# Kernel tuning notes

Hardware: AMD Instinct MI355X
Metric: run time of the kernel (lower is better)

Reference implementation:

```python
import jax, jax.numpy as jnp
from jax import lax
import numpy as np

D_IN = 512    # inputdim
HID = 128     # hiddendim
D_INNER = 2 * HID   # 256
D_PROJ = 2 * D_INNER  # 512
N_STATE = 16
R_DT = 8      # ceil(128/16)
B, H, W = 8, 32, 32


def _layernorm(y, g, b):
    mu = y.mean(-1, keepdims=True)
    var = ((y - mu) ** 2).mean(-1, keepdims=True)
    return (y - mu) / jnp.sqrt(var + 1e-5) * g + b


def _ssm(x, xw, dtw, dtb, Al, Dv, g, be):
    # x: [B, D, L] -> y: [B, L, D]  (Mamba selective scan, delta_softplus=True)
    Bb, D, L = x.shape
    n = Al.shape[1]
    xd = jnp.einsum('bdl,kd->blk', x, xw)             # [B,L,R+2N]
    dts = xd[..., :R_DT]
    Bs = xd[..., R_DT:R_DT + n]                        # [B,L,N]
    Cs = xd[..., R_DT + n:]                            # [B,L,N]
    delta = jax.nn.softplus(jnp.einsum('blr,dr->bld', dts, dtw) + dtb)  # [B,L,D]
    A = -jnp.exp(Al)                                   # [D,N]
    xt = x.transpose(0, 2, 1)                          # [B,L,D]
    dA = jnp.exp(delta[..., None] * A)                 # [B,L,D,N]
    dBx = delta[..., None] * Bs[:, :, None, :] * xt[..., None]  # [B,L,D,N]

    def step(h, inp):
        da, dbx, c = inp
        h = h * da + dbx
        return h, jnp.einsum('bdn,bn->bd', h, c)

    h0 = jnp.zeros((Bb, D, n), x.dtype)
    _, ys = lax.scan(step, h0, (dA.transpose(1, 0, 2, 3),
                                dBx.transpose(1, 0, 2, 3),
                                Cs.transpose(1, 0, 2)))
    y = ys.transpose(1, 0, 2) + xt * Dv                # [B,L,D]
    return _layernorm(y, g, be)


def _up2(y, h, w):
    Bb, L, C = y.shape
    img = y.transpose(0, 2, 1).reshape(Bb, C, h, w)
    img = jnp.repeat(jnp.repeat(img, 2, axis=2), 2, axis=3)
    return img.reshape(Bb, C, 4 * L).transpose(0, 2, 1)


def _conv1x1(x, w, b):
    return jnp.einsum('bchw,oc->bohw', x, w) + b[None, :, None, None]


def _conv2s2(x, w, b):
    out = lax.conv_general_dilated(x, w, (2, 2), 'VALID',
                                   dimension_numbers=('NCHW', 'OIHW', 'NCHW'))
    return out + b[None, :, None, None]


def _forward(input_f, in_w, in_b, c1_w, c1_b, c2_w, c2_b, c3_w, c3_b, out_w, out_b,
             xw1, dtw1, dtb1, Al1, Dv1, g1, be1,
             xw2, dtw2, dtb2, Al2, Dv2, g2, be2,
             xw3, dtw3, dtb3, Al3, Dv3, g3, be3):
    xz = _conv1x1(input_f, in_w, in_b)
    x, z = jnp.split(xz, 2, axis=1)
    f1 = _conv1x1(x, c1_w, c1_b)                      # [B,256,H,W]
    f2 = _conv2s2(f1, c2_w, c2_b)                     # [B,256,H/2,W/2]
    f3 = _conv2s2(f2, c3_w, c3_b)                     # [B,256,H/4,W/4]

    Bb, C, h3, w3 = f3.shape
    fx3 = f3.reshape(Bb, C, h3 * w3)
    y3 = _ssm(fx3, xw3, dtw3, dtb3, Al3, Dv3, g3, be3) + \
         jnp.flip(_ssm(jnp.flip(fx3, -1), xw3, dtw3, dtb3, Al3, Dv3, g3, be3), 1)
    y2_ = _up2(y3, h3, w3)

    _, _, h2, w2 = f2.shape
    fx2 = f2.reshape(Bb, C, h2 * w2)
    y2 = _ssm(fx2, xw2, dtw2, dtb2, Al2, Dv2, g2, be2) + \
         jnp.flip(_ssm(jnp.flip(fx2, -1), xw2, dtw2, dtb2, Al2, Dv2, g2, be2), 1) + y2_
    y1_ = _up2(y2, h2, w2)

    _, _, h1, w1 = f1.shape
    fx1 = f1.reshape(Bb, C, h1 * w1)
    # NOTE: source uses fssm1 forward and fssm2 on the flipped sequence
    y1 = _ssm(fx1, xw1, dtw1, dtb1, Al1, Dv1, g1, be1) + \
         jnp.flip(_ssm(jnp.flip(fx1, -1), xw2, dtw2, dtb2, Al2, Dv2, g2, be2), 1) + y1_

    out1 = y1.transpose(0, 2, 1).reshape(Bb, C, h1, w1)
    out = out1 * jax.nn.silu(z)
    return _conv1x1(out, out_w, out_b)


def setup_inputs() -> dict:
    key = jax.random.key(0)
    ks = iter(jax.random.split(key, 64))
    def nrm(shape, s=0.05):
        return (jax.random.normal(next(ks), shape, dtype=jnp.float32) * s)
    inp = {
        'input_f': jax.random.normal(next(ks), (B, D_IN, H, W), dtype=jnp.float32),
        'in_w': nrm((D_PROJ, D_IN)), 'in_b': nrm((D_PROJ,)),
        'c1_w': nrm((D_INNER, D_INNER)), 'c1_b': nrm((D_INNER,)),
        'c2_w': nrm((D_INNER, D_INNER, 2, 2)), 'c2_b': nrm((D_INNER,)),
        'c3_w': nrm((D_INNER, D_INNER, 2, 2)), 'c3_b': nrm((D_INNER,)),
        'out_w': nrm((D_IN, D_INNER)), 'out_b': nrm((D_IN,)),
    }
    Al = jnp.log(jnp.tile(jnp.arange(1, N_STATE + 1, dtype=jnp.float32), (D_INNER, 1)))
    for i in (1, 2, 3):
        inp[f'xw{i}'] = nrm((R_DT + 2 * N_STATE, D_INNER))
        inp[f'dtw{i}'] = nrm((D_INNER, R_DT), s=R_DT ** -0.5)
        inp[f'dtb{i}'] = nrm((D_INNER,)) - 4.0   # inv-softplus of small dt
        inp[f'Al{i}'] = Al
        inp[f'Dv{i}'] = jnp.ones((D_INNER,), jnp.float32)
        inp[f'g{i}'] = jnp.ones((D_INNER,), jnp.float32)
        inp[f'be{i}'] = jnp.zeros((D_INNER,), jnp.float32)
    return inp


def reference(input_f, in_w, in_b, c1_w, c1_b, c2_w, c2_b, c3_w, c3_b, out_w, out_b,
              xw1, dtw1, dtb1, Al1, Dv1, g1, be1,
              xw2, dtw2, dtb2, Al2, Dv2, g2, be2,
              xw3, dtw3, dtb3, Al3, Dv3, g3, be3):
    return _forward(input_f, in_w, in_b, c1_w, c1_b, c2_w, c2_b, c3_w, c3_b, out_w, out_b,
                    xw1, dtw1, dtb1, Al1, Dv1, g1, be1,
                    xw2, dtw2, dtb2, Al2, Dv2, g2, be2,
                    xw3, dtw3, dtb3, Al3, Dv3, g3, be3)
```

## Files before the change

### kernel.cpp

```cpp
#include <hip/hip_runtime.h>
#include <cstddef>

#define DEV static __device__ __forceinline__

typedef __attribute__((ext_vector_type(8))) short short8;
typedef __attribute__((ext_vector_type(4))) float floatx4;

DEV float siluf(float v) { return v / (1.f + expf(-v)); }

DEV unsigned short f2bf(float f) {
  unsigned int u = __float_as_uint(f);
  u += 0x7fff + ((u >> 16) & 1);
  return (unsigned short)(u >> 16);
}
DEV float bf2f(unsigned short u) {
  return __uint_as_float(((unsigned int)u) << 16);
}
DEV float4 bf2f4(ushort4 v) {
  return make_float4(bf2f(v.x), bf2f(v.y), bf2f(v.z), bf2f(v.w));
}

template <int CTRL>
DEV float qadd(float v) {
  int s = __builtin_amdgcn_update_dpp(__float_as_int(v), __float_as_int(v),
                                      CTRL, 0xF, 0xF, false);
  return v + __int_as_float(s);
}

__global__ __launch_bounds__(256) void prep_k(
    const float* __restrict__ in_w, const float* __restrict__ c1_w,
    const float* __restrict__ c2_w, const float* __restrict__ c3_w,
    const float* __restrict__ out_w, const float* __restrict__ xw1,
    const float* __restrict__ xw2, const float* __restrict__ xw3,
    unsigned short* __restrict__ wsW,
    const float* __restrict__ input_f, unsigned short* __restrict__ inT)
{
  __shared__ float tile[32][33];
  int bid = blockIdx.x;
  int t = threadIdx.x;
  if (bid < 3960) {
    int gid = bid * 256 + t;
    float v;
    if      (gid < 262144)  v = in_w[gid];
    else if (gid < 327680)  v = c1_w[gid - 262144];
    else if (gid < 589824)  {
      int off = gid - 327680;
      int o = off >> 10, kk = off & 1023, ij = kk >> 8, c = kk & 255;
      v = c2_w[o * 1024 + c * 4 + ij];
    }
    else if (gid < 851968)  {
      int off = gid - 589824;
      int o = off >> 10, kk = off & 1023, ij = kk >> 8, c = kk & 255;
      v = c3_w[o * 1024 + c * 4 + ij];
    }
    else if (gid < 983040)  v = out_w[gid - 851968];
    else if (gid < 993280)  v = xw1[gid - 983040];
    else if (gid < 1003520) v = xw2[gid - 993280];
    else                    v = xw3[gid - 1003520];
    wsW[gid] = f2bf(v);
  } else {
    int idx = bid - 3960;
    int b = idx >> 9, blk = idx & 511;
    int pt = blk & 31, ct = blk >> 5;
    int p0 = pt * 32, c0 = ct * 32;
    int r = t >> 5, cc = t & 31;
#pragma unroll
    for (int i = 0; i < 4; i++) {
      int row = r + 8 * i;
      tile[row][cc] = input_f[((size_t)b * 512 + c0 + row) * 1024 + p0 + cc];
    }
    __syncthreads();
#pragma unroll
    for (int i = 0; i < 4; i++) {
      int row = r + 8 * i;
      inT[((size_t)b * 1024 + p0 + row) * 512 + c0 + cc] = f2bf(tile[cc][row]);
    }
  }
}

template <int EPI>
DEV void mgemm_body(const unsigned short* __restrict__ A, long long sA,
                    const unsigned short* __restrict__ B, long long sB,
                    const float* __restrict__ bias,
                    void* __restrict__ O1, void* __restrict__ O2,
                    int M, int N, int K, int Mt, int Nt, int bid)
{
  __shared__ __align__(16) unsigned short Ab[2 * 128 * 40];
  __shared__ __align__(16) unsigned short Bb[2 * 128 * 40];
  int tiles = Mt * Nt;
  int bb = bid / tiles;
  int rr = bid - bb * tiles;
  int m0 = (rr / Nt) * 128;
  int n0 = (rr % Nt) * 128;
  const unsigned short* Ap = A + (size_t)bb * sA;
  const unsigned short* Bp = B + (size_t)bb * sB;

  int t = threadIdx.x;
  int lane = t & 63;
  int wm = ((t >> 7) & 1) * 64;
  int wn = ((t >> 6) & 1) * 64;
  int l15 = lane & 15, quad = lane >> 4;

  int srow = t >> 1;
  int shalf = (t & 1) * 16;
  int arow = m0 + srow; if (arow > M - 1) arow = M - 1;
  int brow = n0 + srow; if (brow > N - 1) brow = N - 1;
  const unsigned short* ap = Ap + (size_t)arow * K + shalf;
  const unsigned short* bp = Bp + (size_t)brow * K + shalf;
  unsigned short* as = &Ab[srow * 40 + shalf];
  unsigned short* bs = &Bb[srow * 40 + shalf];

  floatx4 acc[4][4] = {};

  uint4 a0 = *(const uint4*)(ap);
  uint4 a1 = *(const uint4*)(ap + 8);
  uint4 b0 = *(const uint4*)(bp);
  uint4 b1 = *(const uint4*)(bp + 8);
// ... 3 lines not shown
  int cur = 0;
  for (int k0 = 0; k0 < K; k0 += 32) {
    bool last = (k0 + 32 >= K);
    if (!last) {
      a0 = *(const uint4*)(ap + k0 + 32);
      a1 = *(const uint4*)(ap + k0 + 40);
      b0 = *(const uint4*)(bp + k0 + 32);
      b1 = *(const uint4*)(bp + k0 + 40);
    }
    int co = cur * 5120;
    short8 af[4], bfr[4];
#pragma unroll
    for (int i = 0; i < 4; i++)
      af[i] = *(const short8*)&Ab[co + (wm + i * 16 + l15) * 40 + quad * 8];
#pragma unroll
    for (int j = 0; j < 4; j++)
      bfr[j] = *(const short8*)&Bb[co + (wn + j * 16 + l15) * 40 + quad * 8];
#pragma unroll
    for (int i = 0; i < 4; i++)
#pragma unroll
      for (int j = 0; j < 4; j++)
        acc[i][j] = __builtin_amdgcn_mfma_f32_16x16x32_bf16(af[i], bfr[j],
                                                            acc[i][j], 0, 0, 0);
    if (!last) {
      int no = 5120 - co;
      *(uint4*)(as + no) = a0; *(uint4*)(as + no + 8) = a1;
      *(uint4*)(bs + no) = b0; *(uint4*)(bs + no + 8) = b1;
      __syncthreads();
      cur ^= 1;
    }
  }

  if (EPI == 1) {
    unsigned short* Yt = (unsigned short*)O1;
    unsigned short* Ys = (unsigned short*)O2;
    float bn[4]; int nn[4];
#pragma unroll
    for (int j = 0; j < 4; j++) { nn[j] = n0 + wn + j * 16 + l15; bn[j] = bias[nn[j]]; }
#pragma unroll
    for (int i = 0; i < 4; i++) {
      int pixb = m0 + wm + i * 16 + quad * 4;
#pragma unroll
      for (int j = 0; j < 4; j++) {
        int n = nn[j];
        if (n < 256) {
#pragma unroll
          for (int r = 0; r < 4; r++)
            Yt[((size_t)bb * 1024 + pixb + r) * 256 + n] = f2bf(acc[i][j][r] + bn[j]);
        } else {
#pragma unroll
          for (int r = 0; r < 4; r++)
            Ys[((size_t)bb * 1024 + pixb + r) * 256 + (n - 256)] =
                f2bf(siluf(acc[i][j][r] + bn[j]));
        }
      }
    }
  } else {
#pragma unroll
    for (int i = 0; i < 4; i++) {
      int m = m0 + wm + i * 16 + quad * 4;
#pragma unroll
      for (int j = 0; j < 4; j++) {
        int n = n0 + wn + j * 16 + l15;
        if (m < M && n < N) {
          float vr[4];
#pragma unroll
          for (int r = 0; r < 4; r++)
            vr[r] = acc[i][j][r] + (bias ? bias[m + r] : 0.f);
          if (EPI == 0) {
            float* Y0 = (float*)O1;
            float* yp = &Y0[((size_t)bb * M + m) * N + n];
#pragma unroll
            for (int r = 0; r < 4; r++) yp[(size_t)r * N] = vr[r];
          } else {
            unsigned short* Y0b = (unsigned short*)O1;
            unsigned short* Yt  = (unsigned short*)O2;
#pragma unroll
            for (int r = 0; r < 4; r++)
              Y0b[((size_t)bb * M + m + r) * N + n] = f2bf(vr[r]);
            ushort4 o;
            o.x = f2bf(vr[0]); o.y = f2bf(vr[1]); o.z = f2bf(vr[2]); o.w = f2bf(vr[3]);
            *(ushort4*)&Yt[((size_t)bb * N + n) * M + m] = o;
          }
        }
      }
    }
  }
}

template <int EPI>
__global__ __launch_bounds__(256) void mgemm_k(
    const unsigned short* __restrict__ A, long long sA,
    const unsigned short* __restrict__ B, long long sB,
    const float* __restrict__ bias, void* __restrict__ O1, void* __restrict__ O2,
    int M, int N, int K, int Mt, int Nt)
{
  mgemm_body<EPI>(A, sA, B, sB, bias, O1, O2, M, N, K, Mt, Nt, blockIdx.x);
}

__global__ __launch_bounds__(256) void cgemm_k(
    const unsigned short* __restrict__ A,
    const unsigned short* __restrict__ B, long long sB,
    const float* __restrict__ bias,
    unsigned short* __restrict__ O1, unsigned short* __restrict__ O2,
    int M, int N, int K, int Mt, int Nt)
{
  __shared__ __align__(16) unsigned short Ab[2][64 * 72];
  __shared__ __align__(16) unsigned short Bb[2][32 * 72];
  int bid = blockIdx.x;
  int tiles = Mt * Nt;
  int bb = bid / tiles;
  int rr = bid - bb * tiles;
  int m0 = (rr / Nt) * 64;
  int n0 = (rr % Nt) * 32;
  const unsigned short* Bp = B + (size_t)bb * sB;

  int t = threadIdx.x, lane = t & 63;
  int wm = ((t >> 7) & 1) * 32;
  int wn = ((t >> 6) & 1) * 16;
  int l15 = lane & 15, quad = lane >> 4;

  int ar = t >> 2, ac = (t & 3) * 16;
  int brc = (t >> 2) & 31, bc = (t & 3) * 16;
  const unsigned short* apc = A + (size_t)(m0 + ar) * K + ac;
  const unsigned short* bpc = Bp + (size_t)(n0 + brc) * K + bc;

  floatx4 acc2[2] = {};

  uint4 av0 = *(const uint4*)(apc);
  uint4 av1 = *(const uint4*)(apc + 8);
// ... 39 lines not shown
      unsigned short* asn = &Ab[cur ^ 1][0] + ar * 72 + ac;
      *(uint4*)asn = av0; *(uint4*)(asn + 8) = av1;
      if (t < 128) {
        unsigned short* bsn = &Bb[cur ^ 1][0] + brc * 72 + bc;
        *(uint4*)bsn = bv0; *(uint4*)(bsn + 8) = bv1;
      }
      __syncthreads();
      cur ^= 1;
    }
  }

#pragma unroll
  for (int i = 0; i < 2; i++) {
    int m = m0 + wm + i * 16 + quad * 4;
    int n = n0 + wn + l15;
    float vr[4];
#pragma unroll
    for (int r = 0; r < 4; r++) vr[r] = acc2[i][r] + bias[m + r];
#pragma unroll
    for (int r = 0; r < 4; r++)
      O1[((size_t)bb * M + m + r) * N + n] = f2bf(vr[r]);
    ushort4 o;
    o.x = f2bf(vr[0]); o.y = f2bf(vr[1]); o.z = f2bf(vr[2]); o.w = f2bf(vr[3]);
    *(ushort4*)&O2[((size_t)bb * N + n) * M + m] = o;
  }
}

__global__ __launch_bounds__(256) void fat1_k(
    const unsigned short* __restrict__ w_xw12, const unsigned short* __restrict__ f1t,
    float* __restrict__ xd12, unsigned short* __restrict__ ic2)
{
  int bid = blockIdx.x;
  if (bid < 64) {
    mgemm_body<0>(w_xw12, 0, f1t, 1024 * 256, nullptr, xd12, nullptr,
                  80, 1024, 256, 1, 8, bid);
  } else {
    int idx = (bid - 64) * 256 + threadIdx.x;
    int cs = idx & 31, ij = (idx >> 5) & 3, n = (idx >> 7) & 255, b = idx >> 15;
    int i = ij >> 1, j = ij & 1;
    int y = n >> 4, x = n & 15;
    int pix = (2 * y + i) * 32 + 2 * x + j;
    uint4 v = *(const uint4*)&f1t[((size_t)b * 1024 + pix) * 256 + cs * 8];
    *(uint4*)&ic2[((size_t)b * 256 + n) * 1024 + ij * 256 + cs * 8] = v;
  }
}

__global__ __launch_bounds__(256) void fat2_k(
    const unsigned short* __restrict__ w_xw2, const unsigned short* __restrict__ f2t,
    float* __restrict__ xd2, unsigned short* __restrict__ ic3)
{
  int bid = blockIdx.x;
  if (bid < 16) {
    mgemm_body<0>(w_xw2, 0, f2t, 256 * 256, nullptr, xd2, nullptr,
                  40, 256, 256, 1, 2, bid);
  } else {
    int idx = (bid - 16) * 256 + threadIdx.x;
    int cs = idx & 31, ij = (idx >> 5) & 3, n = (idx >> 7) & 63, b = idx >> 13;
    int i = ij >> 1, j = ij & 1;
    int y = n >> 3, x = n & 7;
    int pix = (2 * y + i) * 16 + 2 * x + j;
    uint4 v = *(const uint4*)&f2t[((size_t)b * 256 + pix) * 256 + cs * 8];
    *(uint4*)&ic3[((size_t)b * 64 + n) * 1024 + ij * 256 + cs * 8] = v;
  }
}

__global__ __launch_bounds__(256) void post_all_k(
    const float* __restrict__ xd12, const float* __restrict__ xd2,
    const float* __restrict__ xd3,
    const float* __restrict__ dtw1, const float* __restrict__ dtb1,
    const float* __restrict__ dtw2, const float* __restrict__ dtb2,
    const float* __restrict__ dtw3, const float* __restrict__ dtb3,
    float* __restrict__ d1f, float* __restrict__ bc1f,
    float* __restrict__ d1b, float* __restrict__ bc1b,
    float* __restrict__ d2g, float* __restrict__ bc2,
    float* __restrict__ d3g, float* __restrict__ bc3)
{
  int bid = blockIdx.x;
  const float* xd; int bstride, L; const float *dtw, *dtb; float *dg, *bg;
  int lt, b;
  if (bid < 512) {
    int r = bid; lt = r & 63; b = r >> 6;
    xd = xd12; bstride = 80 * 1024; L = 1024; dtw = dtw1; dtb = dtb1; dg = d1f; bg = bc1f;
  } else if (bid < 1024) {
    int r = bid - 512; lt = r & 63; b = r >> 6;
    xd = xd12 + 40 * 1024; bstride = 80 * 1024; L = 1024; dtw = dtw2; dtb = dtb2; dg = d1b; bg = bc1b;
  } else if (bid < 1152) {
// ... 14 lines not shown
    int tt = t - 128;
    int c = tt >> 2, seg = tt & 3;
    float4 v = *(const float4*)&xb[(size_t)(8 + c) * L + seg * 4];
    *(float4*)&bg[((size_t)b * 32 + c) * L + l0 + seg * 4] = v;
  }
  __syncthreads();
  int d = t;
  float dtwv[8];
#pragma unroll
  for (int r = 0; r < 8; r++) dtwv[r] = dtw[d * 8 + r];
  float dtbv = dtb[d];
  float spv[16];
#pragma unroll
  for (int l = 0; l < 16; l++) {
    float s = dtbv;
#pragma unroll
    for (int r = 0; r < 8; r++) s += dl[r][l] * dtwv[r];
    spv[l] = fmaxf(s, 0.f) + log1pf(expf(-fabsf(s)));
  }
  float* dout = dg + ((size_t)b * 256 + d) * L + l0;
#pragma unroll
  for (int i = 0; i < 4; i++)
    *(float4*)&dout[4 * i] = make_float4(spv[4 * i], spv[4 * i + 1],
                                         spv[4 * i + 2], spv[4 * i + 3]);
}

#define SCAN_STEPA(DVV, DXV, BVV) {                     \
    float e_ = __builtin_amdgcn_exp2f((DVV) * A2);      \
    h = h * e_ + (BVV) * (DXV);                         \
    S += (DVV); }

__global__ __launch_bounds__(256) void scanA_k(
    const unsigned short* __restrict__ f1b, const unsigned short* __restrict__ f2b,
    const float* __restrict__ d1f, const float* __restrict__ bc1f,
    const float* __restrict__ d1b, const float* __restrict__ bc1b,
    const float* __restrict__ d2,  const float* __restrict__ bc2,
    const float* __restrict__ Al1, const float* __restrict__ Al2,
    float* __restrict__ cP, float* __restrict__ cQ)
{
  __shared__ __align__(16) float lds[48][68];
  int bid = blockIdx.x;
  int sid, tseg, L; const unsigned short* xin; const float *dlp, *bcp, *Alp;
  if (bid < 4096) {
    sid = bid >> 4; tseg = bid & 15; L = 1024; xin = f1b;
    if (((sid >> 4) & 1) == 0) { dlp = d1f; bcp = bc1f; Alp = Al1; }
    else                       { dlp = d1b; bcp = bc1b; Alp = Al2; }
  } else {
    int idx = bid - 4096; sid = idx >> 2; tseg = idx & 3; L = 256;
    xin = f2b; dlp = d2; bcp = bc2; Alp = Al2;
  }
  int b = sid >> 5, dir = (sid >> 4) & 1, g = sid & 15;
  int t = threadIdx.x, n = t & 15, dloc = t >> 4, d = g * 16 + dloc;
  int mbase = dir ? (L - 64 * (tseg + 1)) : 64 * tseg;

  int r0 = t >> 4, cs = t & 15;
  {
    const float* p0 = dlp + ((size_t)b * 256 + g * 16 + r0) * L + mbase;
    const unsigned short* p1 = xin + ((size_t)b * 256 + g * 16 + r0) * L + mbase;
    const float* p2 = bcp + ((size_t)b * 32 + r0) * L + mbase;
    float4 v0 = *(const float4*)(p0 + cs * 4);
    float4 xf = bf2f4(*(const ushort4*)(p1 + cs * 4));
    float4 v2 = *(const float4*)(p2 + cs * 4);
    float4 dx = make_float4(v0.x * xf.x, v0.y * xf.y, v0.z * xf.z, v0.w * xf.w);
    *(float4*)&lds[r0][cs * 4]      = v0;
    *(float4*)&lds[16 + r0][cs * 4] = dx;
    *(float4*)&lds[32 + r0][cs * 4] = v2;
  }
  __syncthreads();

  float A2 = -expf(Alp[d * 16 + n]) * 1.442695040888963f;
  float h = 0.f, S = 0.f;
  if (dir == 0) {
#pragma unroll
    for (int g4 = 0; g4 < 16; g4++) {
      int cb = 4 * g4;
      float4 dv4 = *(const float4*)&lds[dloc][cb];
      float4 dx4 = *(const float4*)&lds[16 + dloc][cb];
      float4 bv4 = *(const float4*)&lds[32 + n][cb];
      SCAN_STEPA(dv4.x, dx4.x, bv4.x);
      SCAN_STEPA(dv4.y, dx4.y, bv4.y);
      SCAN_STEPA(dv4.z, dx4.z, bv4.z);
      SCAN_STEPA(dv4.w, dx4.w, bv4.w);
    }
  } else {
#pragma unroll
    for (int g4 = 0; g4 < 16; g4++) {
      int cb = 60 - 4 * g4;
      float4 dv4 = *(const float4*)&lds[dloc][cb];
      float4 dx4 = *(const float4*)&lds[16 + dloc][cb];
      float4 bv4 = *(const float4*)&lds[32 + n][cb];
      SCAN_STEPA(dv4.w, dx4.w, bv4.w);
      SCAN_STEPA(dv4.z, dx4.z, bv4.z);
      SCAN_STEPA(dv4.y, dx4.y, bv4.y);
      SCAN_STEPA(dv4.x, dx4.x, bv4.x);
    }
  }
  cP[(size_t)bid * 256 + t] = __builtin_amdgcn_exp2f(S * A2);
  cQ[(size_t)bid * 256 + t] = h;
}

#define QSTEP(DS, XU, CI, II) {                                         \
    float4 bv = *(const float4*)&ld_b[CI][n0];                          \
    float4 cv = *(const float4*)&ld_c[CI][n0];                          \
    float xs_ = bf2f(XU) * (DS);                                        \
    float4 e_;                                                          \
    e_.x = __builtin_amdgcn_exp2f((DS) * A4.x);                         \
    e_.y = __builtin_amdgcn_exp2f((DS) * A4.y);                         \
    e_.z = __builtin_amdgcn_exp2f((DS) * A4.z);                         \
    e_.w = __builtin_amdgcn_exp2f((DS) * A4.w);                         \
    h4.x = h4.x * e_.x + bv.x * xs_;                                    \
    h4.y = h4.y * e_.y + bv.y * xs_;                                    \
    h4.z = h4.z * e_.z + bv.z * xs_;                                    \
    h4.w = h4.w * e_.w + bv.w * xs_;                                    \
    float pp_ = h4.x * cv.x + h4.y * cv.y + h4.z * cv.z + h4.w * cv.w;  \
    pp_ = qadd<0xB1>(pp_);                                              \
    pp_ = qadd<0x4E>(pp_);                                              \
    ysel = (nq == (II)) ? pp_ : ysel; }

DEV float4 pcomb(float4 P, float4 h, float4 Q) {
  return make_float4(P.x * h.x + Q.x, P.y * h.y + Q.y,
                     P.z * h.z + Q.z, P.w * h.w + Q.w);
}

__global__ __launch_bounds__(256) void scanC_k(
    const unsigned short* __restrict__ f1b, const unsigned short* __restrict__ f2b,
    const unsigned short* __restrict__ f3b,
    const float* __restrict__ d1f, const float* __restrict__ bc1f,
    const float* __restrict__ d1b, const float* __restrict__ bc1b,
    const float* __restrict__ d2,  const float* __restrict__ bc2,
    const float* __restrict__ d3,  const float* __restrict__ bc3,
    float* __restrict__ y1f, float* __restrict__ y1b,
    float* __restrict__ y2f, float* __restrict__ y2b,
    float* __restrict__ y3f, float* __restrict__ y3b,
    const float* __restrict__ Al1, const float* __restrict__ Dv1,
    const float* __restrict__ Al2, const float* __restrict__ Dv2,
    const float* __restrict__ Al3, const float* __restrict__ Dv3,
    const float* __restrict__ cP, const float* __restrict__ cQ)
{
  __shared__ __align__(16) float ld_d[64][68];
  __shared__ __align__(16) unsigned short ld_xs[64][72];
  __shared__ __align__(16) float ld_b[64][20];
  __shared__ __align__(16) float ld_c[64][20];

  int bid = blockIdx.x;
  int b, dir, g4, tseg, L, lvl;
  const unsigned short* xin; const float *dlp, *bcp, *Alp, *Dvp; float* yo;
  if (bid < 1024) {
    b = bid >> 7; dir = (bid >> 6) & 1; g4 = (bid >> 4) & 3; tseg = bid & 15;
    L = 1024; xin = f1b; lvl = 1;
    if (dir == 0) { dlp = d1f; bcp = bc1f; Alp = Al1; Dvp = Dv1; yo = y1f; }
    else          { dlp = d1b; bcp = bc1b; Alp = Al2; Dvp = Dv2; yo = y1b; }
  } else if (bid < 1280) {
    int idx = bid - 1024;
    b = idx >> 5; dir = (idx >> 4) & 1; g4 = (idx >> 2) & 3; tseg = idx & 3;
    L = 256; xin = f2b; lvl = 2;
    dlp = d2; bcp = bc2; Alp = Al2; Dvp = Dv2; yo = dir ? y2b : y2f;
  } else {
    int idx = bid - 1280;
    b = idx >> 3; dir = (idx >> 2) & 1; g4 = idx & 3; tseg = 0;
    L = 64; xin = f3b; lvl = 3;
    dlp = d3; bcp = bc3; Alp = Al3; Dvp = Dv3; yo = dir ? y3b : y3f;
  }
  int mbase = dir ? (L - 64 * (tseg + 1)) : 64 * tseg;
  int t = threadIdx.x;
  int dl = t >> 2, nq = t & 3, n0 = nq * 4;
  int d = g4 * 64 + dl;

  {
    int rr = t >> 2, q = t & 3;
    const float* dr = dlp + ((size_t)b * 256 + g4 * 64 + rr) * L + mbase;
    const unsigned short* xr = xin + ((size_t)b * 256 + g4 * 64 + rr) * L + mbase;
#pragma unroll
    for (int j = 0; j < 4; ++j) {
      int c = q * 4 + 16 * j;
      float4 dv = *(const float4*)(dr + c);
      ushort4 xu = *(const ushort4*)(xr + c);
      *(float4*)&ld_d[rr][c] = dv;
      *(ushort4*)&ld_xs[rr][c] = xu;
    }
    int nn = t >> 4, c4 = t & 15;
    const float* br = bcp + ((size_t)b * 32 + nn) * L + mbase + c4 * 4;
    const float* cr = br + (size_t)16 * L;
    float4 bv = *(const float4*)br;
    float4 cv = *(const float4*)cr;
    ld_b[c4 * 4 + 0][nn] = bv.x; ld_b[c4 * 4 + 1][nn] = bv.y;
    ld_b[c4 * 4 + 2][nn] = bv.z; ld_b[c4 * 4 + 3][nn] = bv.w;
    ld_c[c4 * 4 + 0][nn] = cv.x; ld_c[c4 * 4 + 1][nn] = cv.y;
    ld_c[c4 * 4 + 2][nn] = cv.z; ld_c[c4 * 4 + 3][nn] = cv.w;
  }

  float4 A4;
  A4.x = -expf(Alp[d * 16 + n0 + 0]) * 1.442695040888963f;
  A4.y = -expf(Alp[d * 16 + n0 + 1]) * 1.442695040888963f;
  A4.z = -expf(Alp[d * 16 + n0 + 2]) * 1.442695040888963f;
  A4.w = -expf(Alp[d * 16 + n0 + 3]) * 1.442695040888963f;
  float Dvv = Dvp[d];

  float4 h4 = make_float4(0.f, 0.f, 0.f, 0.f);
  if (tseg > 0) {
    int gold = g4 * 4 + (dl >> 4);
    int soff = (lvl == 1) ? (b * 32 + dir * 16 + gold) * 16
                          : 4096 + (b * 32 + dir * 16 + gold) * 4;
    size_t cbase = (size_t)soff * 256 + (size_t)((dl & 15) * 16 + n0);
    int s = 0;
    for (; s + 4 <= tseg; s += 4) {
      const float* p = &cP[cbase + (size_t)s * 256];
      const float* q = &cQ[cbase + (size_t)s * 256];
      float4 P0 = *(const float4*)(p);       float4 Q0 = *(const float4*)(q);
      float4 P1 = *(const float4*)(p + 256); float4 Q1 = *(const float4*)(q + 256);
      float4 P2 = *(const float4*)(p + 512); float4 Q2 = *(const float4*)(q + 512);
      float4 P3 = *(const float4*)(p + 768); float4 Q3 = *(const float4*)(q + 768);
      h4 = pcomb(P0, h4, Q0); h4 = pcomb(P1, h4, Q1);
      h4 = pcomb(P2, h4, Q2); h4 = pcomb(P3, h4, Q3);
    }
    for (; s < tseg; ++s) {
      float4 P = *(const float4*)&cP[cbase + (size_t)s * 256];
      float4 Q = *(const float4*)&cQ[cbase + (size_t)s * 256];
      h4 = pcomb(P, h4, Q);
    }
  }
  __syncthreads();

  float* ybase = yo + ((size_t)b * L + mbase) * 256 + d;
  if (dir == 0) {
#pragma unroll
    for (int p = 0; p < 4; ++p) {
      float yk[4];
#pragma unroll
      for (int j = 0; j < 4; ++j) {
        int cb = 16 * p + 4 * j;
        float4 dv4 = *(const float4*)&ld_d[dl][cb];
        ushort4 xu4 = *(const ushort4*)&ld_xs[dl][cb];
        float ysel = 0.f;
        QSTEP(dv4.x, xu4.x, cb + 0, 0);
        QSTEP(dv4.y, xu4.y, cb + 1, 1);
        QSTEP(dv4.z, xu4.z, cb + 2, 2);
        QSTEP(dv4.w, xu4.w, cb + 3, 3);
        yk[j] = ysel;
      }
#pragma unroll
      for (int j = 0; j < 4; ++j) {
        int cst = 16 * p + 4 * j + nq;
        float xv = bf2f(ld_xs[dl][cst]);
        ybase[(size_t)cst * 256] = yk[j] + xv * Dvv;
      }
    }
  } else {
#pragma unroll
    for (int p = 0; p < 4; ++p) {
      float yk[4];
#pragma unroll
      for (int j = 0; j < 4; ++j) {
        int cb = 60 - 16 * p - 4 * j;
        float4 dv4 = *(const float4*)&ld_d[dl][cb];
        ushort4 xu4 = *(const ushort4*)&ld_xs[dl][cb];
        float ysel = 0.f;
        QSTEP(dv4.w, xu4.w, cb + 3, 0);
        QSTEP(dv4.z, xu4.z, cb + 2, 1);
        QSTEP(dv4.y, xu4.y, cb + 1, 2);
        QSTEP(dv4.x, xu4.x, cb + 0, 3);
        yk[j] = ysel;
      }
#pragma unroll
      for (int j = 0; j < 4; ++j) {
        int cst = 60 - 16 * p - 4 * j + (3 - nq);
        float xv = bf2f(ld_xs[dl][cst]);
        ybase[(size_t)cst * 256] = yk[j] + xv * Dvv;
      }
    }
  }
}

template <int OUTBF>
__global__ __launch_bounds__(256) void ln_combine(
    const float* __restrict__ yf, const float* __restrict__ yb,
    const float* __restrict__ gf, const float* __restrict__ bef,
    const float* __restrict__ gb, const float* __restrict__ beb,
    const float* __restrict__ up, int Wc,
    const unsigned short* __restrict__ szb, void* __restrict__ outv,
    int L, int Lsh, int Wfsh)
{
  int t = threadIdx.x;
  int row = blockIdx.x * 4 + (t >> 6);
  int lane = t & 63;
  int b = row >> Lsh, l = row & (L - 1);
  size_t base = (size_t)row * 256 + lane * 4;
  float4 vf = *(const float4*)&yf[base];
  float4 vb = *(const float4*)&yb[base];
  float4 s;
  s.x = vf.x + vf.y + vf.z + vf.w;
  s.y = vf.x * vf.x + vf.y * vf.y + vf.z * vf.z + vf.w * vf.w;
  s.z = vb.x + vb.y + vb.z + vb.w;
  s.w = vb.x * vb.x + vb.y * vb.y + vb.z * vb.z + vb.w * vb.w;
#pragma unroll
  for (int m = 1; m < 64; m <<= 1) {
    s.x += __shfl_xor(s.x, m);
    s.y += __shfl_xor(s.y, m);
    s.z += __shfl_xor(s.z, m);
// ... 43 lines not shown
  const float* c1_w  = (const float*)d_in[3];
  const float* c1_b  = (const float*)d_in[4];
  const float* c2_w  = (const float*)d_in[5];
  const float* c2_b  = (const float*)d_in[6];
  const float* c3_w  = (const float*)d_in[7];
  const float* c3_b  = (const float*)d_in[8];
  const float* out_w = (const float*)d_in[9];
  const float* out_b = (const float*)d_in[10];
  const float* xw1  = (const float*)d_in[11];
  const float* dtw1 = (const float*)d_in[12];
  const float* dtb1 = (const float*)d_in[13];
  const float* Al1  = (const float*)d_in[14];
  const float* Dv1  = (const float*)d_in[15];
  const float* g1   = (const float*)d_in[16];
  const float* be1  = (const float*)d_in[17];
  const float* xw2  = (const float*)d_in[18];
  const float* dtw2 = (const float*)d_in[19];
  const float* dtb2 = (const float*)d_in[20];
  const float* Al2  = (const float*)d_in[21];
  const float* Dv2  = (const float*)d_in[22];
  const float* g2   = (const float*)d_in[23];
  const float* be2  = (const float*)d_in[24];
  const float* xw3  = (const float*)d_in[25];
  const float* dtw3 = (const float*)d_in[26];
  const float* dtb3 = (const float*)d_in[27];
  const float* Al3  = (const float*)d_in[28];
  const float* Dv3  = (const float*)d_in[29];
  const float* g3   = (const float*)d_in[30];
  const float* be3  = (const float*)d_in[31];

  float* ws = (float*)d_ws;
  constexpr size_t M1 = 2097152;
  float* d1f = ws;
  unsigned short* xt = (unsigned short*)(ws + M1);
  float* y1f = ws + M1;
  unsigned short* szb = (unsigned short*)(ws + 2 * M1);
  unsigned short* f1b = (unsigned short*)(ws + 3 * M1);
  unsigned short* G = (unsigned short*)(ws + 3 * M1) + 2097152;
  float* d1b = ws + 4 * M1;
  unsigned short* inT = (unsigned short*)(ws + 5 * M1);
  unsigned short* ic2 = inT;
  unsigned short* f1t = inT + 2097152;
  unsigned short* ic3 = f1t;
  float* y1b = ws + 5 * M1;
  size_t o = 6 * M1;
  unsigned short* f2b = (unsigned short*)(ws + o); o += 524288;
  unsigned short* f3b = (unsigned short*)(ws + o); o += 131072;
  float* bc1f = ws + o; o += 262144;
  float* bc1b = ws + o; o += 262144;
  float* d2   = ws + o; o += 524288;
  float* bc2  = ws + o; o += 65536;
  float* d3   = ws + o; o += 131072;
  float* bc3  = ws + o; o += 16384;
  float* y2f  = ws + o; o += 524288;
  float* y2b  = ws + o; o += 524288;
  float* y3f  = ws + o; o += 131072;
  float* y3b  = ws + o; o += 131072;
  float* y3c  = ws + o; o += 131072;
  float* y2c  = ws + o; o += 524288;
  float* cP   = ws + o; o += 1310720;
  float* cQ   = ws + o; o += 1310720;
  unsigned short* wsW = (unsigned short*)(ws + o); o += 506880;
  float* xd12 = cP;
  float* xd2  = cP + 655360;
  float* xd3  = cP + 737280;
  unsigned short* f2t = (unsigned short*)cQ;
  unsigned short* f3t = (unsigned short*)(cQ + 262144);
  unsigned short* w_in   = wsW;
  unsigned short* w_c1   = wsW + 262144;
  unsigned short* w_c2   = wsW + 327680;
  unsigned short* w_c3   = wsW + 589824;
  unsigned short* w_out  = wsW + 851968;
  unsigned short* w_xw12 = wsW + 983040;
  unsigned short* w_xw2  = wsW + 993280;
  unsigned short* w_xw3  = wsW + 1003520;

  dim3 blk(256);

  prep_k<<<dim3(8056), blk, 0, stream>>>(in_w, c1_w, c2_w, c3_w, out_w,
                                         xw1, xw2, xw3, wsW, input_f, inT);
  mgemm_k<1><<<dim3(256), blk, 0, stream>>>(inT, 1024 * 512, w_in, 0, in_b,
                                            xt, szb, 1024, 512, 512, 8, 4);
  mgemm_k<3><<<dim3(128), blk, 0, stream>>>(w_c1, 0, xt, 1024 * 256, c1_b,
                                            f1b, f1t, 256, 1024, 256, 2, 8);
  fat1_k<<<dim3(1088), blk, 0, stream>>>(w_xw12, f1t, xd12, ic2);
  cgemm_k<<<dim3(256), blk, 0, stream>>>(w_c2, ic2, 256 * 1024, c2_b,
                                         f2b, f2t, 256, 256, 1024, 4, 8);
  fat2_k<<<dim3(272), blk, 0, stream>>>(w_xw2, f2t, xd2, ic3);
  cgemm_k<<<dim3(64), blk, 0, stream>>>(w_c3, ic3, 64 * 1024, c3_b,
                                        f3b, f3t, 256, 64, 1024, 4, 2);
  mgemm_k<0><<<dim3(8), blk, 0, stream>>>(w_xw3, 0, f3t, 64 * 256, nullptr,
                                          xd3, nullptr, 40, 64, 256, 1, 1);
  post_all_k<<<dim3(1184), blk, 0, stream>>>(xd12, xd2, xd3,
                                             dtw1, dtb1, dtw2, dtb2, dtw3, dtb3,
                                             d1f, bc1f, d1b, bc1b, d2, bc2, d3, bc3);
  scanA_k<<<dim3(5120), blk, 0, stream>>>(f1b, f2b, d1f, bc1f, d1b, bc1b,
                                          d2, bc2, Al1, Al2, cP, cQ);
  scanC_k<<<dim3(1344), blk, 0, stream>>>(f1b, f2b, f3b,
                                          d1f, bc1f, d1b, bc1b, d2, bc2, d3, bc3,
                                          y1f, y1b, y2f, y2b, y3f, y3b,
                                          Al1, Dv1, Al2, Dv2, Al3, Dv3, cP, cQ);
  ln_combine<0><<<dim3(128), blk, 0, stream>>>(y3f, y3b, g3, be3, g3, be3,
                                               nullptr, 0, nullptr, y3c, 64, 6, 3);
  ln_combine<0><<<dim3(512), blk, 0, stream>>>(y2f, y2b, g2, be2, g2, be2,
                                               y3c, 8, nullptr, y2c, 256, 8, 4);
  ln_combine<1><<<dim3(2048), blk, 0, stream>>>(y1f, y1b, g1, be1, g2, be2,
                                                y2c, 16, szb, G, 1024, 10, 5);
  mgemm_k<0><<<dim3(256), blk, 0, stream>>>(w_out, 0, G, 1024 * 256, out_b,
                                            (float*)d_out, nullptr,
                                            512, 1024, 256, 4, 8);
}
```

Measured before the change: 316.6 us.

## Fold 1x1 conv into input projection and halve scan chunk length

Precomputes the product of the c1 conv weight and the x half of the input projection weight, plus a folded bias, inside the prep kernel. This lets a single GEMM emit f1 directly in both layouts and removes the separate c1 GEMM launch. Separately, scan segments shrink from 64 to 32 timesteps, doubling scanA/scanC blocks, and level 3 is now chunked too, to raise parallelism. The trade-offs are larger carry buffers, longer sequential prefix combines in scanC, and bf16 rounding of the fused weight that changes numerics slightly.

```diff
diff --git a/kernel.cpp b/kernel.cpp
--- a/kernel.cpp
+++ b/kernel.cpp
@@ -33,9 +33,13 @@
     const float* __restrict__ out_w, const float* __restrict__ xw1,
     const float* __restrict__ xw2, const float* __restrict__ xw3,
     unsigned short* __restrict__ wsW,
-    const float* __restrict__ input_f, unsigned short* __restrict__ inT)
+    const float* __restrict__ input_f, unsigned short* __restrict__ inT,
+    const float* __restrict__ in_b, const float* __restrict__ c1_b,
+    unsigned short* __restrict__ w_fz, float* __restrict__ bias_fz)
 {
   __shared__ float tile[32][33];
+  __shared__ float c1s[1024];
+  __shared__ float part[32][8];
   int bid = blockIdx.x;
   int t = threadIdx.x;
   if (bid < 3960) {
@@ -58,7 +62,7 @@
     else if (gid < 1003520) v = xw2[gid - 993280];
     else                    v = xw3[gid - 1003520];
     wsW[gid] = f2bf(v);
-  } else {
+  } else if (bid < 8056) {
     int idx = bid - 3960;
     int b = idx >> 9, blk = idx & 511;
     int pt = blk & 31, ct = blk >> 5;
@@ -75,6 +79,48 @@
       int row = r + 8 * i;
       inT[((size_t)b * 1024 + p0 + row) * 512 + c0 + cc] = f2bf(tile[cc][row]);
     }
+  } else if (bid < 8184) {
+    int ib = bid - 8056;
+    int ot = ib >> 1;
+    int ci = ((ib & 1) << 8) + t;
+#pragma unroll
+    for (int rr = 0; rr < 4; rr++)
+      c1s[rr * 256 + t] = c1_w[(size_t)(ot * 4 + rr) * 256 + t];
+    __syncthreads();
+    float acc[4] = {0.f, 0.f, 0.f, 0.f};
+#pragma unroll 4
+    for (int m = 0; m < 256; m++) {
+      float wv = in_w[(size_t)m * 512 + ci];
+#pragma unroll
+      for (int rr = 0; rr < 4; rr++) acc[rr] += c1s[rr * 256 + m] * wv;
+    }
+#pragma unroll
+    for (int rr = 0; rr < 4; rr++)
+      w_fz[(size_t)(ot * 4 + rr) * 512 + ci] = f2bf(acc[rr]);
+  } else if (bid < 8192) {
+    int jb = bid - 8184;
+    int oo = t >> 3, mc = t & 7;
+    int o = jb * 32 + oo;
+    float s = 0.f;
+#pragma unroll 8
+    for (int mm = 0; mm < 32; mm++) {
+      int m = mc * 32 + mm;
+      s += c1_w[(size_t)o * 256 + m] * in_b[m];
+    }
+    part[oo][mc] = s;
+    __syncthreads();
+    if (mc == 0) {
+      float a = c1_b[o];
+#pragma unroll
+      for (int k = 0; k < 8; k++) a += part[oo][k];
+      bias_fz[o] = a;
+    }
+    if (jb == 0) bias_fz[256 + t] = in_b[256 + t];
+  } else {
+    int r = bid - 8192;
+    const float* src = in_w + (size_t)(256 + r) * 512;
+    w_fz[(size_t)(256 + r) * 512 + t]       = f2bf(src[t]);
+    w_fz[(size_t)(256 + r) * 512 + 256 + t] = f2bf(src[256 + t]);
   }
 }
 
@@ -83,6 +129,7 @@
                     const unsigned short* __restrict__ B, long long sB,
                     const float* __restrict__ bias,
                     void* __restrict__ O1, void* __restrict__ O2,
+                    void* __restrict__ O3,
                     int M, int N, int K, int Mt, int Nt, int bid)
 {
   __shared__ __align__(16) unsigned short Ab[2 * 128 * 40];
@@ -152,8 +199,9 @@
   }
 
   if (EPI == 1) {
-    unsigned short* Yt = (unsigned short*)O1;
-    unsigned short* Ys = (unsigned short*)O2;
+    unsigned short* F1t = (unsigned short*)O1;
+    unsigned short* F1b = (unsigned short*)O2;
+    unsigned short* Sz  = (unsigned short*)O3;
     float bn[4]; int nn[4];
 #pragma unroll
     for (int j = 0; j < 4; j++) { nn[j] = n0 + wn + j * 16 + l15; bn[j] = bias[nn[j]]; }
@@ -163,15 +211,21 @@
 #pragma unroll
       for (int j = 0; j < 4; j++) {
         int n = nn[j];
+        float vr[4];
+#pragma unroll
+        for (int r = 0; r < 4; r++) vr[r] = acc[i][j][r] + bn[j];
         if (n < 256) {
 #pragma unroll
           for (int r = 0; r < 4; r++)
-            Yt[((size_t)bb * 1024 + pixb + r) * 256 + n] = f2bf(acc[i][j][r] + bn[j]);
+            F1t[((size_t)bb * 1024 + pixb + r) * 256 + n] = f2bf(vr[r]);
+          ushort4 o4;
+          o4.x = f2bf(vr[0]); o4.y = f2bf(vr[1]); o4.z = f2bf(vr[2]); o4.w = f2bf(vr[3]);
+          *(ushort4*)&F1b[((size_t)bb * 256 + n) * 1024 + pixb] = o4;
         } else {
 #pragma unroll
           for (int r = 0; r < 4; r++)
-            Ys[((size_t)bb * 1024 + pixb + r) * 256 + (n - 256)] =
-                f2bf(siluf(acc[i][j][r] + bn[j]));
+            Sz[((size_t)bb * 1024 + pixb + r) * 256 + (n - 256)] =
+                f2bf(siluf(vr[r]));
         }
       }
     }
@@ -187,21 +241,10 @@
 #pragma unroll
           for (int r = 0; r < 4; r++)
             vr[r] = acc[i][j][r] + (bias ? bias[m + r] : 0.f);
-          if (EPI == 0) {
-            float* Y0 = (float*)O1;
-            float* yp = &Y0[((size_t)bb * M + m) * N + n];
-#pragma unroll
-            for (int r = 0; r < 4; r++) yp[(size_t)r * N] = vr[r];
-          } else {
-            unsigned short* Y0b = (unsigned short*)O1;
-            unsigned short* Yt  = (unsigned short*)O2;
-#pragma unroll
-            for (int r = 0; r < 4; r++)
-              Y0b[((size_t)bb * M + m + r) * N + n] = f2bf(vr[r]);
-            ushort4 o;
-            o.x = f2bf(vr[0]); o.y = f2bf(vr[1]); o.z = f2bf(vr[2]); o.w = f2bf(vr[3]);
-            *(ushort4*)&Yt[((size_t)bb * N + n) * M + m] = o;
-          }
+          float* Y0 = (float*)O1;
+          float* yp = &Y0[((size_t)bb * M + m) * N + n];
+#pragma unroll
+          for (int r = 0; r < 4; r++) yp[(size_t)r * N] = vr[r];
         }
       }
     }
@@ -213,9 +256,10 @@
     const unsigned short* __restrict__ A, long long sA,
     const unsigned short* __restrict__ B, long long sB,
     const float* __restrict__ bias, void* __restrict__ O1, void* __restrict__ O2,
+    void* __restrict__ O3,
     int M, int N, int K, int Mt, int Nt)
 {
-  mgemm_body<EPI>(A, sA, B, sB, bias, O1, O2, M, N, K, Mt, Nt, blockIdx.x);
+  mgemm_body<EPI>(A, sA, B, sB, bias, O1, O2, O3, M, N, K, Mt, Nt, blockIdx.x);
 }
 
 __global__ __launch_bounds__(256) void cgemm_k(
@@ -321,7 +365,7 @@
 {
   int bid = blockIdx.x;
   if (bid < 64) {
-    mgemm_body<0>(w_xw12, 0, f1t, 1024 * 256, nullptr, xd12, nullptr,
+    mgemm_body<0>(w_xw12, 0, f1t, 1024 * 256, nullptr, xd12, nullptr, nullptr,
                   80, 1024, 256, 1, 8, bid);
   } else {
     int idx = (bid - 64) * 256 + threadIdx.x;
@@ -340,7 +384,7 @@
 {
   int bid = blockIdx.x;
   if (bid < 16) {
-    mgemm_body<0>(w_xw2, 0, f2t, 256 * 256, nullptr, xd2, nullptr,
+    mgemm_body<0>(w_xw2, 0, f2t, 256 * 256, nullptr, xd2, nullptr, nullptr,
                   40, 256, 256, 1, 2, bid);
   } else {
     int idx = (bid - 16) * 256 + threadIdx.x;
@@ -421,38 +465,46 @@
 
 __global__ __launch_bounds__(256) void scanA_k(
     const unsigned short* __restrict__ f1b, const unsigned short* __restrict__ f2b,
+    const unsigned short* __restrict__ f3b,
     const float* __restrict__ d1f, const float* __restrict__ bc1f,
     const float* __restrict__ d1b, const float* __restrict__ bc1b,
     const float* __restrict__ d2,  const float* __restrict__ bc2,
+    const float* __restrict__ d3,  const float* __restrict__ bc3,
     const float* __restrict__ Al1, const float* __restrict__ Al2,
+    const float* __restrict__ Al3,
     float* __restrict__ cP, float* __restrict__ cQ)
 {
-  __shared__ __align__(16) float lds[48][68];
+  __shared__ __align__(16) float lds[48][36];
   int bid = blockIdx.x;
   int sid, tseg, L; const unsigned short* xin; const float *dlp, *bcp, *Alp;
-  if (bid < 4096) {
-    sid = bid >> 4; tseg = bid & 15; L = 1024; xin = f1b;
+  if (bid < 8192) {
+    sid = bid >> 5; tseg = bid & 31; L = 1024; xin = f1b;
     if (((sid >> 4) & 1) == 0) { dlp = d1f; bcp = bc1f; Alp = Al1; }
     else                       { dlp = d1b; bcp = bc1b; Alp = Al2; }
-  } else {
-    int idx = bid - 4096; sid = idx >> 2; tseg = idx & 3; L = 256;
+  } else if (bid < 10240) {
+    int idx = bid - 8192; sid = idx >> 3; tseg = idx & 7; L = 256;
     xin = f2b; dlp = d2; bcp = bc2; Alp = Al2;
+  } else {
+    int idx = bid - 10240; sid = idx >> 1; tseg = idx & 1; L = 64;
+    xin = f3b; dlp = d3; bcp = bc3; Alp = Al3;
   }
   int b = sid >> 5, dir = (sid >> 4) & 1, g = sid & 15;
   int t = threadIdx.x, n = t & 15, dloc = t >> 4, d = g * 16 + dloc;
-  int mbase = dir ? (L - 64 * (tseg + 1)) : 64 * tseg;
-
-  int r0 = t >> 4, cs = t & 15;
-  {
+  int mbase = dir ? (L - 32 * (tseg + 1)) : 32 * tseg;
+
+  if (t < 128) {
+    int r0 = t >> 3, cs = t & 7;
     const float* p0 = dlp + ((size_t)b * 256 + g * 16 + r0) * L + mbase;
     const unsigned short* p1 = xin + ((size_t)b * 256 + g * 16 + r0) * L + mbase;
-    const float* p2 = bcp + ((size_t)b * 32 + r0) * L + mbase;
     float4 v0 = *(const float4*)(p0 + cs * 4);
     float4 xf = bf2f4(*(const ushort4*)(p1 + cs * 4));
-    float4 v2 = *(const float4*)(p2 + cs * 4);
     float4 dx = make_float4(v0.x * xf.x, v0.y * xf.y, v0.z * xf.z, v0.w * xf.w);
     *(float4*)&lds[r0][cs * 4]      = v0;
     *(float4*)&lds[16 + r0][cs * 4] = dx;
+  } else {
+    int r0 = (t - 128) >> 3, cs = t & 7;
+    const float* p2 = bcp + ((size_t)b * 32 + r0) * L + mbase;
+    float4 v2 = *(const float4*)(p2 + cs * 4);
     *(float4*)&lds[32 + r0][cs * 4] = v2;
   }
   __syncthreads();
@@ -461,7 +513,7 @@
   float h = 0.f, S = 0.f;
   if (dir == 0) {
 #pragma unroll
-    for (int g4 = 0; g4 < 16; g4++) {
+    for (int g4 = 0; g4 < 8; g4++) {
       int cb = 4 * g4;
       float4 dv4 = *(const float4*)&lds[dloc][cb];
       float4 dx4 = *(const float4*)&lds[16 + dloc][cb];
@@ -473,8 +525,8 @@
     }
   } else {
 #pragma unroll
-    for (int g4 = 0; g4 < 16; g4++) {
-      int cb = 60 - 4 * g4;
+    for (int g4 = 0; g4 < 8; g4++) {
+      int cb = 28 - 4 * g4;
       float4 dv4 = *(const float4*)&lds[dloc][cb];
       float4 dx4 = *(const float4*)&lds[16 + dloc][cb];
       float4 bv4 = *(const float4*)&lds[32 + n][cb];
@@ -526,31 +578,31 @@
     const float* __restrict__ Al3, const float* __restrict__ Dv3,
     const float* __restrict__ cP, const float* __restrict__ cQ)
 {
-  __shared__ __align__(16) float ld_d[64][68];
-  __shared__ __align__(16) unsigned short ld_xs[64][72];
-  __shared__ __align__(16) float ld_b[64][20];
-  __shared__ __align__(16) float ld_c[64][20];
+  __shared__ __align__(16) float ld_d[64][36];
+  __shared__ __align__(16) unsigned short ld_xs[64][40];
+  __shared__ __align__(16) float ld_b[32][20];
+  __shared__ __align__(16) float ld_c[32][20];
 
   int bid = blockIdx.x;
   int b, dir, g4, tseg, L, lvl;
   const unsigned short* xin; const float *dlp, *bcp, *Alp, *Dvp; float* yo;
-  if (bid < 1024) {
-    b = bid >> 7; dir = (bid >> 6) & 1; g4 = (bid >> 4) & 3; tseg = bid & 15;
+  if (bid < 2048) {
+    b = bid >> 8; dir = (bid >> 7) & 1; g4 = (bid >> 5) & 3; tseg = bid & 31;
     L = 1024; xin = f1b; lvl = 1;
     if (dir == 0) { dlp = d1f; bcp = bc1f; Alp = Al1; Dvp = Dv1; yo = y1f; }
     else          { dlp = d1b; bcp = bc1b; Alp = Al2; Dvp = Dv2; yo = y1b; }
-  } else if (bid < 1280) {
-    int idx = bid - 1024;
-    b = idx >> 5; dir = (idx >> 4) & 1; g4 = (idx >> 2) & 3; tseg = idx & 3;
+  } else if (bid < 2560) {
+    int idx = bid - 2048;
+    b = idx >> 6; dir = (idx >> 5) & 1; g4 = (idx >> 3) & 3; tseg = idx & 7;
     L = 256; xin = f2b; lvl = 2;
     dlp = d2; bcp = bc2; Alp = Al2; Dvp = Dv2; yo = dir ? y2b : y2f;
   } else {
-    int idx = bid - 1280;
-    b = idx >> 3; dir = (idx >> 2) & 1; g4 = idx & 3; tseg = 0;
+    int idx = bid - 2560;
+    b = idx >> 4; dir = (idx >> 3) & 1; g4 = (idx >> 1) & 3; tseg = idx & 1;
     L = 64; xin = f3b; lvl = 3;
     dlp = d3; bcp = bc3; Alp = Al3; Dvp = Dv3; yo = dir ? y3b : y3f;
   }
-  int mbase = dir ? (L - 64 * (tseg + 1)) : 64 * tseg;
+  int mbase = dir ? (L - 32 * (tseg + 1)) : 32 * tseg;
   int t = threadIdx.x;
   int dl = t >> 2, nq = t & 3, n0 = nq * 4;
   int d = g4 * 64 + dl;
@@ -560,22 +612,27 @@
     const float* dr = dlp + ((size_t)b * 256 + g4 * 64 + rr) * L + mbase;
     const unsigned short* xr = xin + ((size_t)b * 256 + g4 * 64 + rr) * L + mbase;
 #pragma unroll
-    for (int j = 0; j < 4; ++j) {
+    for (int j = 0; j < 2; ++j) {
       int c = q * 4 + 16 * j;
       float4 dv = *(const float4*)(dr + c);
       ushort4 xu = *(const ushort4*)(xr + c);
       *(float4*)&ld_d[rr][c] = dv;
       *(ushort4*)&ld_xs[rr][c] = xu;
     }
-    int nn = t >> 4, c4 = t & 15;
-    const float* br = bcp + ((size_t)b * 32 + nn) * L + mbase + c4 * 4;
-    const float* cr = br + (size_t)16 * L;
-    float4 bv = *(const float4*)br;
-    float4 cv = *(const float4*)cr;
-    ld_b[c4 * 4 + 0][nn] = bv.x; ld_b[c4 * 4 + 1][nn] = bv.y;
-    ld_b[c4 * 4 + 2][nn] = bv.z; ld_b[c4 * 4 + 3][nn] = bv.w;
-    ld_c[c4 * 4 + 0][nn] = cv.x; ld_c[c4 * 4 + 1][nn] = cv.y;
-    ld_c[c4 * 4 + 2][nn] = cv.z; ld_c[c4 * 4 + 3][nn] = cv.w;
+    if (t < 128) {
+      int nn = t >> 3, c4 = t & 7;
+      const float* br = bcp + ((size_t)b * 32 + nn) * L + mbase + c4 * 4;
+      float4 bv = *(const float4*)br;
+      ld_b[c4 * 4 + 0][nn] = bv.x; ld_b[c4 * 4 + 1][nn] = bv.y;
+      ld_b[c4 * 4 + 2][nn] = bv.z; ld_b[c4 * 4 + 3][nn] = bv.w;
+    } else {
+      int tt = t - 128;
+      int nn = tt >> 3, c4 = tt & 7;
+      const float* cr = bcp + ((size_t)b * 32 + 16 + nn) * L + mbase + c4 * 4;
+      float4 cv = *(const float4*)cr;
+      ld_c[c4 * 4 + 0][nn] = cv.x; ld_c[c4 * 4 + 1][nn] = cv.y;
+      ld_c[c4 * 4 + 2][nn] = cv.z; ld_c[c4 * 4 + 3][nn] = cv.w;
+    }
   }
 
   float4 A4;
@@ -588,8 +645,9 @@
   float4 h4 = make_float4(0.f, 0.f, 0.f, 0.f);
   if (tseg > 0) {
     int gold = g4 * 4 + (dl >> 4);
-    int soff = (lvl == 1) ? (b * 32 + dir * 16 + gold) * 16
-                          : 4096 + (b * 32 + dir * 16 + gold) * 4;
+    int soff = (lvl == 1) ? (b * 32 + dir * 16 + gold) * 32
+             : (lvl == 2) ? 8192 + (b * 32 + dir * 16 + gold) * 8
+                          : 10240 + (b * 32 + dir * 16 + gold) * 2;
     size_t cbase = (size_t)soff * 256 + (size_t)((dl & 15) * 16 + n0);
     int s = 0;
     for (; s + 4 <= tseg; s += 4) {
@@ -613,7 +671,7 @@
   float* ybase = yo + ((size_t)b * L + mbase) * 256 + d;
   if (dir == 0) {
 #pragma unroll
-    for (int p = 0; p < 4; ++p) {
+    for (int p = 0; p < 2; ++p) {
       float yk[4];
 #pragma unroll
       for (int j = 0; j < 4; ++j) {
@@ -636,11 +694,11 @@
     }
   } else {
 #pragma unroll
-    for (int p = 0; p < 4; ++p) {
+    for (int p = 0; p < 2; ++p) {
       float yk[4];
 #pragma unroll
       for (int j = 0; j < 4; ++j) {
-        int cb = 60 - 16 * p - 4 * j;
+        int cb = 28 - 16 * p - 4 * j;
         float4 dv4 = *(const float4*)&ld_d[dl][cb];
         ushort4 xu4 = *(const ushort4*)&ld_xs[dl][cb];
         float ysel = 0.f;
@@ -652,7 +710,7 @@
       }
 #pragma unroll
       for (int j = 0; j < 4; ++j) {
-        int cst = 60 - 16 * p - 4 * j + (3 - nq);
+        int cst = 28 - 16 * p - 4 * j + (3 - nq);
         float xv = bf2f(ld_xs[dl][cst]);
         ybase[(size_t)cst * 256] = yk[j] + xv * Dvv;
       }
@@ -762,7 +820,7 @@
   float* ws = (float*)d_ws;
   constexpr size_t M1 = 2097152;
   float* d1f = ws;
-  unsigned short* xt = (unsigned short*)(ws + M1);
+  unsigned short* f1t = (unsigned short*)(ws + M1);
   float* y1f = ws + M1;
   unsigned short* szb = (unsigned short*)(ws + 2 * M1);
   unsigned short* f1b = (unsigned short*)(ws + 3 * M1);
@@ -770,8 +828,7 @@
   float* d1b = ws + 4 * M1;
   unsigned short* inT = (unsigned short*)(ws + 5 * M1);
   unsigned short* ic2 = inT;
-  unsigned short* f1t = inT + 2097152;
-  unsigned short* ic3 = f1t;
+  unsigned short* ic3 = inT + 2097152;
   float* y1b = ws + 5 * M1;
   size_t o = 6 * M1;
   unsigned short* f2b = (unsigned short*)(ws + o); o += 524288;
@@ -788,16 +845,16 @@
   float* y3b  = ws + o; o += 131072;
   float* y3c  = ws + o; o += 131072;
   float* y2c  = ws + o; o += 524288;
-  float* cP   = ws + o; o += 1310720;
-  float* cQ   = ws + o; o += 1310720;
+  float* cP   = ws + o; o += 2752512;
+  float* cQ   = ws + o; o += 2752512;
   unsigned short* wsW = (unsigned short*)(ws + o); o += 506880;
+  float* bias_fz = ws + o; o += 512;
+  unsigned short* w_fz = (unsigned short*)(ws + o); o += 131072;
   float* xd12 = cP;
   float* xd2  = cP + 655360;
   float* xd3  = cP + 737280;
   unsigned short* f2t = (unsigned short*)cQ;
   unsigned short* f3t = (unsigned short*)(cQ + 262144);
-  unsigned short* w_in   = wsW;
-  unsigned short* w_c1   = wsW + 262144;
   unsigned short* w_c2   = wsW + 327680;
   unsigned short* w_c3   = wsW + 589824;
   unsigned short* w_out  = wsW + 851968;
@@ -807,12 +864,11 @@
 
   dim3 blk(256);
 
-  prep_k<<<dim3(8056), blk, 0, stream>>>(in_w, c1_w, c2_w, c3_w, out_w,
-                                         xw1, xw2, xw3, wsW, input_f, inT);
-  mgemm_k<1><<<dim3(256), blk, 0, stream>>>(inT, 1024 * 512, w_in, 0, in_b,
-                                            xt, szb, 1024, 512, 512, 8, 4);
-  mgemm_k<3><<<dim3(128), blk, 0, stream>>>(w_c1, 0, xt, 1024 * 256, c1_b,
-                                            f1b, f1t, 256, 1024, 256, 2, 8);
+  prep_k<<<dim3(8448), blk, 0, stream>>>(in_w, c1_w, c2_w, c3_w, out_w,
+                                         xw1, xw2, xw3, wsW, input_f, inT,
+                                         in_b, c1_b, w_fz, bias_fz);
+  mgemm_k<1><<<dim3(256), blk, 0, stream>>>(inT, 1024 * 512, w_fz, 0, bias_fz,
+                                            f1t, f1b, szb, 1024, 512, 512, 8, 4);
   fat1_k<<<dim3(1088), blk, 0, stream>>>(w_xw12, f1t, xd12, ic2);
   cgemm_k<<<dim3(256), blk, 0, stream>>>(w_c2, ic2, 256 * 1024, c2_b,
                                          f2b, f2t, 256, 256, 1024, 4, 8);
@@ -820,13 +876,14 @@
   cgemm_k<<<dim3(64), blk, 0, stream>>>(w_c3, ic3, 64 * 1024, c3_b,
                                         f3b, f3t, 256, 64, 1024, 4, 2);
   mgemm_k<0><<<dim3(8), blk, 0, stream>>>(w_xw3, 0, f3t, 64 * 256, nullptr,
-                                          xd3, nullptr, 40, 64, 256, 1, 1);
+                                          xd3, nullptr, nullptr, 40, 64, 256, 1, 1);
   post_all_k<<<dim3(1184), blk, 0, stream>>>(xd12, xd2, xd3,
                                              dtw1, dtb1, dtw2, dtb2, dtw3, dtb3,
                                              d1f, bc1f, d1b, bc1b, d2, bc2, d3, bc3);
-  scanA_k<<<dim3(5120), blk, 0, stream>>>(f1b, f2b, d1f, bc1f, d1b, bc1b,
-                                          d2, bc2, Al1, Al2, cP, cQ);
-  scanC_k<<<dim3(1344), blk, 0, stream>>>(f1b, f2b, f3b,
+  scanA_k<<<dim3(10752), blk, 0, stream>>>(f1b, f2b, f3b,
+                                           d1f, bc1f, d1b, bc1b, d2, bc2, d3, bc3,
+                                           Al1, Al2, Al3, cP, cQ);
+  scanC_k<<<dim3(2688), blk, 0, stream>>>(f1b, f2b, f3b,
                                           d1f, bc1f, d1b, bc1b, d2, bc2, d3, bc3,
                                           y1f, y1b, y2f, y2b, y3f, y3b,
                                           Al1, Dv1, Al2, Dv2, Al3, Dv3, cP, cQ);
@@ -837,6 +894,6 @@
   ln_combine<1><<<dim3(2048), blk, 0, stream>>>(y1f, y1b, g1, be1, g2, be2,
                                                 y2c, 16, szb, G, 1024, 10, 5);
   mgemm_k<0><<<dim3(256), blk, 0, stream>>>(w_out, 0, G, 1024 * 256, out_b,
-                                            (float*)d_out, nullptr,
+                                            (float*)d_out, nullptr, nullptr,
                                             512, 1024, 256, 4, 8);
 }
```

Result: slower. 332.0 us (+4.9%).
